# Performance work log

Measured on AMD Instinct MI355X. Metric: run time of the kernel, lower is better.

The kernel has to match this reference:

```python
import jax, jax.numpy as jnp
import numpy as np


def setup_inputs() -> dict:
    key = jax.random.key(0)
    k1, k2, k3 = jax.random.split(key, 3)
    n, c, h, w = 32, 384, 56, 56
    m, d_model = 8, 768
    x = jax.random.normal(k1, (n, c, h, w), dtype=jnp.float32)
    global_feature = jax.random.normal(k2, (n, m, d_model), dtype=jnp.float32)
    # Linear(d_model, 2*c): torch weight shape (2c, d_model)
    W_kv = jax.random.normal(k3, (2 * c, d_model), dtype=jnp.float32) * (1.0 / np.sqrt(d_model))
    b_kv = jnp.zeros((2 * c,), dtype=jnp.float32)
    return {"x": x, "global_feature": global_feature, "W_kv": W_kv, "b_kv": b_kv}


def reference(x, global_feature, W_kv, b_kv):
    n, c, h, w = x.shape
    # MLP (single Linear + ReLU6, no BN since bn=False)
    kv = jnp.einsum('nmd,ed->nme', global_feature, W_kv) + b_kv  # [n, m, 2c]
    kv = jnp.clip(kv, 0.0, 6.0)  # ReLU6
    K = kv[:, :, :c]   # [n, m, c]
    V = kv[:, :, c:]   # [n, m, c]
    q = x.reshape(n, c, h * w).transpose(0, 2, 1)  # [n, hw, c]
    scores = jnp.einsum('nqc,nkc->nqk', q, K)       # [n, hw, m] (unscaled)
    attn = jax.nn.softmax(scores, axis=-1)
    v_agg = jnp.einsum('nqk,nkc->nqc', attn, V)     # [n, hw, c]
    feature = v_agg.transpose(0, 2, 1).reshape(n, c, h, w)
    return feature + x
```

## Files before the change

kernel.cpp:

```cpp
#include <hip/hip_runtime.h>


#define NC 384
#define HWP 3136
#define DD 768
#define MM 8
#define EE 768

__global__ __launch_bounds__(256) void kv_kernel(const float* __restrict__ gf,
                                                 const float* __restrict__ Wk,
                                                 const float* __restrict__ bk,
                                                 float* __restrict__ kv) {
    __shared__ float g[MM * DD];
    const int n = blockIdx.y;
    const int et = blockIdx.x;
    const int t = threadIdx.x;

    const float* gfn = gf + (size_t)n * (MM * DD);
    for (int i = t; i < MM * DD; i += 256) g[i] = gfn[i];
    __syncthreads();

    const int e = et * 128 + (t & 127);
    const int mb = (t >> 7) * 4;

    const float4* w4 = (const float4*)(Wk + (size_t)e * DD);
    const float4* g0 = (const float4*)(g + (mb + 0) * DD);
    const float4* g1 = (const float4*)(g + (mb + 1) * DD);
    const float4* g2 = (const float4*)(g + (mb + 2) * DD);
    const float4* g3 = (const float4*)(g + (mb + 3) * DD);

    float a0 = 0.f, a1 = 0.f, a2 = 0.f, a3 = 0.f;
    #pragma unroll 8
    for (int i = 0; i < DD / 4; ++i) {
        const float4 w = w4[i];
        const float4 v0 = g0[i];
        const float4 v1 = g1[i];
        const float4 v2 = g2[i];
        const float4 v3 = g3[i];
        a0 += w.x * v0.x + w.y * v0.y + w.z * v0.z + w.w * v0.w;
        a1 += w.x * v1.x + w.y * v1.y + w.z * v1.z + w.w * v1.w;
        a2 += w.x * v2.x + w.y * v2.y + w.z * v2.z + w.w * v2.w;
        a3 += w.x * v3.x + w.y * v3.y + w.z * v3.z + w.w * v3.w;
    }
    const float bv = bk[e];
    float* o = kv + (size_t)n * (MM * EE);
    o[(mb + 0) * EE + e] = fminf(fmaxf(a0 + bv, 0.f), 6.f);
    o[(mb + 1) * EE + e] = fminf(fmaxf(a1 + bv, 0.f), 6.f);
    o[(mb + 2) * EE + e] = fminf(fmaxf(a2 + bv, 0.f), 6.f);
    o[(mb + 3) * EE + e] = fminf(fmaxf(a3 + bv, 0.f), 6.f);
}

__global__ __launch_bounds__(256) void attn_kernel(const float* __restrict__ x,
                                                   const float* __restrict__ kv,
                                                   float* __restrict__ out) {
    __shared__ float kvs[MM * EE];
    __shared__ float sc[8][4][64];
    __shared__ float attn_s[8][64];

    const int n = blockIdx.y;
    const int tile = blockIdx.x;
    const int t = threadIdx.x;
    const int p = t & 63;
    const int chunk = t >> 6;
    const int pos = tile * 64 + p;
    const int c0 = chunk * 96;

    const float* kvn = kv + (size_t)n * (MM * EE);
    for (int i = t; i < MM * EE; i += 256) kvs[i] = kvn[i];

    const float* xp = x + (size_t)n * NC * HWP + (size_t)c0 * HWP + pos;
    float xr[96];
    #pragma unroll
    for (int i = 0; i < 96; ++i) xr[i] = xp[(size_t)i * HWP];

    __syncthreads();

    float acc[8];
    #pragma unroll
    for (int k = 0; k < 8; ++k) acc[k] = 0.f;
    #pragma unroll
    for (int i = 0; i < 96; i += 4) {
        #pragma unroll
        for (int k = 0; k < 8; ++k) {
            const float4 kk = *(const float4*)&kvs[k * EE + c0 + i];
            acc[k] += xr[i] * kk.x + xr[i + 1] * kk.y + xr[i + 2] * kk.z + xr[i + 3] * kk.w;
        }
    }
    #pragma unroll
    for (int k = 0; k < 8; ++k) sc[k][chunk][p] = acc[k];
    __syncthreads();

    if (t < 64) {
        float s[8];
        float mx = -1e30f;
        #pragma unroll
        for (int k = 0; k < 8; ++k) {
            s[k] = sc[k][0][t] + sc[k][1][t] + sc[k][2][t] + sc[k][3][t];
            mx = fmaxf(mx, s[k]);
        }
        float sum = 0.f;
        #pragma unroll
        for (int k = 0; k < 8; ++k) {
            s[k] = __expf(s[k] - mx);
            sum += s[k];
        }
        const float inv = 1.f / sum;
        #pragma unroll
        for (int k = 0; k < 8; ++k) attn_s[k][t] = s[k] * inv;
    }
    __syncthreads();

    float aw[8];
    #pragma unroll
    for (int k = 0; k < 8; ++k) aw[k] = attn_s[k][p];

    float* op = out + (size_t)n * NC * HWP + (size_t)c0 * HWP + pos;
    #pragma unroll
    for (int i = 0; i < 96; i += 4) {
        float o0 = xr[i], o1 = xr[i + 1], o2 = xr[i + 2], o3 = xr[i + 3];
        #pragma unroll
        for (int k = 0; k < 8; ++k) {
            const float4 vv = *(const float4*)&kvs[k * EE + 384 + c0 + i];
            o0 += aw[k] * vv.x;
            o1 += aw[k] * vv.y;
            o2 += aw[k] * vv.z;
            o3 += aw[k] * vv.w;
        }
        op[(size_t)(i + 0) * HWP] = o0;
        op[(size_t)(i + 1) * HWP] = o1;
        op[(size_t)(i + 2) * HWP] = o2;
        op[(size_t)(i + 3) * HWP] = o3;
    }
}

extern "C" void kernel_launch(void* const* d_in, const int* in_sizes, int n_in,
                              void* d_out, int out_size, void* d_ws, size_t ws_size,
                              hipStream_t stream) {
    const float* x  = (const float*)d_in[0];
    const float* gf = (const float*)d_in[1];
    const float* Wk = (const float*)d_in[2];
    const float* bk = (const float*)d_in[3];
    float* out = (float*)d_out;
    float* kv = (float*)d_ws;

    kv_kernel<<<dim3(6, 32), 256, 0, stream>>>(gf, Wk, bk, kv);
    attn_kernel<<<dim3(49, 32), 256, 0, stream>>>(x, kv, out);
}
```

Measured before the change: 324.3 us.

## Vectorize attention over 4 spatial positions per thread with float4 loads

Measured after the change: 321.6 us. Within noise of the previous version (-0.8%).

```diff
diff --git a/kernel.cpp b/kernel.cpp
--- a/kernel.cpp
+++ b/kernel.cpp
@@ -20,74 +20,89 @@
     for (int i = t; i < MM * DD; i += 256) g[i] = gfn[i];
     __syncthreads();
 
-    const int e = et * 128 + (t & 127);
-    const int mb = (t >> 7) * 4;
+    const int e = et * 64 + (t & 63);
+    const int mb = (t >> 6) * 2;
 
     const float4* w4 = (const float4*)(Wk + (size_t)e * DD);
     const float4* g0 = (const float4*)(g + (mb + 0) * DD);
     const float4* g1 = (const float4*)(g + (mb + 1) * DD);
-    const float4* g2 = (const float4*)(g + (mb + 2) * DD);
-    const float4* g3 = (const float4*)(g + (mb + 3) * DD);
 
-    float a0 = 0.f, a1 = 0.f, a2 = 0.f, a3 = 0.f;
+    float a0 = 0.f, a1 = 0.f;
     #pragma unroll 8
     for (int i = 0; i < DD / 4; ++i) {
         const float4 w = w4[i];
         const float4 v0 = g0[i];
         const float4 v1 = g1[i];
-        const float4 v2 = g2[i];
-        const float4 v3 = g3[i];
         a0 += w.x * v0.x + w.y * v0.y + w.z * v0.z + w.w * v0.w;
         a1 += w.x * v1.x + w.y * v1.y + w.z * v1.z + w.w * v1.w;
-        a2 += w.x * v2.x + w.y * v2.y + w.z * v2.z + w.w * v2.w;
-        a3 += w.x * v3.x + w.y * v3.y + w.z * v3.z + w.w * v3.w;
     }
     const float bv = bk[e];
     float* o = kv + (size_t)n * (MM * EE);
     o[(mb + 0) * EE + e] = fminf(fmaxf(a0 + bv, 0.f), 6.f);
     o[(mb + 1) * EE + e] = fminf(fmaxf(a1 + bv, 0.f), 6.f);
-    o[(mb + 2) * EE + e] = fminf(fmaxf(a2 + bv, 0.f), 6.f);
-    o[(mb + 3) * EE + e] = fminf(fmaxf(a3 + bv, 0.f), 6.f);
 }
 
 __global__ __launch_bounds__(256) void attn_kernel(const float* __restrict__ x,
                                                    const float* __restrict__ kv,
                                                    float* __restrict__ out) {
     __shared__ float kvs[MM * EE];
-    __shared__ float sc[8][4][64];
+    __shared__ float sc[4][8][64];
     __shared__ float attn_s[8][64];
 
     const int n = blockIdx.y;
     const int tile = blockIdx.x;
     const int t = threadIdx.x;
-    const int p = t & 63;
-    const int chunk = t >> 6;
-    const int pos = tile * 64 + p;
-    const int c0 = chunk * 96;
+    const int p4 = t & 15;
+    const int g = t >> 4;
+    const int w = t >> 6;
+    const int pos0 = tile * 64 + p4 * 4;
+    const int c0 = g * 24;
 
-    const float* kvn = kv + (size_t)n * (MM * EE);
-    for (int i = t; i < MM * EE; i += 256) kvs[i] = kvn[i];
+    const float4* kvn4 = (const float4*)(kv + (size_t)n * (MM * EE));
+    float4* kvs4 = (float4*)kvs;
+    for (int i = t; i < MM * EE / 4; i += 256) kvs4[i] = kvn4[i];
 
-    const float* xp = x + (size_t)n * NC * HWP + (size_t)c0 * HWP + pos;
-    float xr[96];
+    const float* xp = x + (size_t)n * NC * HWP + (size_t)c0 * HWP + pos0;
+    float4 xr[24];
     #pragma unroll
-    for (int i = 0; i < 96; ++i) xr[i] = xp[(size_t)i * HWP];
+    for (int i = 0; i < 24; ++i) xr[i] = *(const float4*)(xp + (size_t)i * HWP);
 
     __syncthreads();
 
-    float acc[8];
+    float acc[8][4];
     #pragma unroll
-    for (int k = 0; k < 8; ++k) acc[k] = 0.f;
+    for (int k = 0; k < 8; ++k)
+        #pragma unroll
+        for (int j = 0; j < 4; ++j) acc[k][j] = 0.f;
+
     #pragma unroll
-    for (int i = 0; i < 96; i += 4) {
+    for (int i = 0; i < 24; ++i) {
+        const float4 xv = xr[i];
         #pragma unroll
         for (int k = 0; k < 8; ++k) {
-            const float4 kk = *(const float4*)&kvs[k * EE + c0 + i];
-            acc[k] += xr[i] * kk.x + xr[i + 1] * kk.y + xr[i + 2] * kk.z + xr[i + 3] * kk.w;
+            const float kc = kvs[k * EE + c0 + i];
+            acc[k][0] += xv.x * kc;
+            acc[k][1] += xv.y * kc;
+            acc[k][2] += xv.z * kc;
+            acc[k][3] += xv.w * kc;
         }
     }
+
     #pragma unroll
-    for (int k = 0; k < 8; ++k) sc[k][chunk][p] = acc[k];
+    for (int k = 0; k < 8; ++k) {
+        #pragma unroll
+        for (int j = 0; j < 4; ++j) {
+            acc[k][j] += __shfl_xor(acc[k][j], 16, 64);
+            acc[k][j] += __shfl_xor(acc[k][j], 32, 64);
+        }
+    }
+    if ((t & 48) == 0) {
+        #pragma unroll
+        for (int k = 0; k < 8; ++k) {
+            *(float4*)&sc[w][k][p4 * 4] =
+                make_float4(acc[k][0], acc[k][1], acc[k][2], acc[k][3]);
+        }
+    }
     __syncthreads();
 
     if (t < 64) {
@@ -95,7 +110,7 @@
         float mx = -1e30f;
         #pragma unroll
         for (int k = 0; k < 8; ++k) {
-            s[k] = sc[k][0][t] + sc[k][1][t] + sc[k][2][t] + sc[k][3][t];
+            s[k] = sc[0][k][t] + sc[1][k][t] + sc[2][k][t] + sc[3][k][t];
             mx = fmaxf(mx, s[k]);
         }
         float sum = 0.f;
@@ -110,26 +125,23 @@
     }
     __syncthreads();
 
-    float aw[8];
+    float4 aw[8];
     #pragma unroll
-    for (int k = 0; k < 8; ++k) aw[k] = attn_s[k][p];
+    for (int k = 0; k < 8; ++k) aw[k] = *(const float4*)&attn_s[k][p4 * 4];
 
-    float* op = out + (size_t)n * NC * HWP + (size_t)c0 * HWP + pos;
+    float* op = out + (size_t)n * NC * HWP + (size_t)c0 * HWP + pos0;
     #pragma unroll
-    for (int i = 0; i < 96; i += 4) {
-        float o0 = xr[i], o1 = xr[i + 1], o2 = xr[i + 2], o3 = xr[i + 3];
+    for (int i = 0; i < 24; ++i) {
+        float4 o = xr[i];
         #pragma unroll
         for (int k = 0; k < 8; ++k) {
-            const float4 vv = *(const float4*)&kvs[k * EE + 384 + c0 + i];
-            o0 += aw[k] * vv.x;
-            o1 += aw[k] * vv.y;
-            o2 += aw[k] * vv.z;
-            o3 += aw[k] * vv.w;
+            const float v = kvs[k * EE + 384 + c0 + i];
+            o.x += aw[k].x * v;
+            o.y += aw[k].y * v;
+            o.z += aw[k].z * v;
+            o.w += aw[k].w * v;
         }
-        op[(size_t)(i + 0) * HWP] = o0;
-        op[(size_t)(i + 1) * HWP] = o1;
-        op[(size_t)(i + 2) * HWP] = o2;
-        op[(size_t)(i + 3) * HWP] = o3;
+        *(float4*)(op + (size_t)i * HWP) = o;
     }
 }
 
@@ -143,6 +155,6 @@
     float* out = (float*)d_out;
     float* kv = (float*)d_ws;
 
-    kv_kernel<<<dim3(6, 32), 256, 0, stream>>>(gf, Wk, bk, kv);
+    kv_kernel<<<dim3(12, 32), 256, 0, stream>>>(gf, Wk, bk, kv);
     attn_kernel<<<dim3(49, 32), 256, 0, stream>>>(x, kv, out);
 }
```
